# Kernel tuning notes

Measured on AMD Instinct MI355X. Metric: run time of the kernel, lower is better.

The kernel has to match this reference:

```python
import jax, jax.numpy as jnp
import numpy as np

MANTISA_BIT = 8.0  # mantisa_bit init arg


def conv3d(x, w, b, stride=1, pad=1):
    # x: [N,C,D,H,W], w: [O,I,kD,kH,kW]
    out = jax.lax.conv_general_dilated(
        x, w,
        window_strides=(stride, stride, stride),
        padding=[(pad, pad)] * 3,
        dimension_numbers=("NCDHW", "OIDHW", "NCDHW"),
    )
    return out + b.reshape(1, -1, 1, 1, 1)


def bfp_quant(x, ch_exp, m_bits):
    # Block floating point: shared per-channel exponent ch_exp [C],
    # signed mantissa with m_bits total bits. scale = 2^(m-1-exp);
    # q = clip(round(x*scale), -(2^(m-1)-1), 2^(m-1)-1)/scale
    scale = jnp.exp2(m_bits - 1.0 - ch_exp).reshape(1, -1, 1, 1, 1)
    lim = 2.0 ** (m_bits - 1.0) - 1.0
    return jnp.clip(jnp.round(x * scale), -lim, lim) / scale


def setup_inputs() -> dict:
    key = jax.random.key(0)
    ks = jax.random.split(key, 7)
    N, C_in, C_out, T, H, W, K = 8, 64, 64, 16, 56, 56, 3
    x = jax.random.normal(ks[0], (N, C_in, T, H, W), jnp.float32)
    w1 = jax.random.normal(ks[1], (C_out, C_in, K, K, K), jnp.float32) * 0.05
    b1 = jax.random.normal(ks[2], (C_out,), jnp.float32) * 0.05
    w2 = jax.random.normal(ks[3], (C_out, C_out, K, K, K), jnp.float32) * 0.05
    b2 = jax.random.normal(ks[4], (C_out,), jnp.float32) * 0.05
    # offline-optimized per-channel shared exponents (opt_exp_act_list[0], [1])
    exp1 = jax.random.randint(ks[5], (C_out,), 2, 6).astype(jnp.float32)
    exp2 = jax.random.randint(ks[6], (C_out,), 2, 6).astype(jnp.float32)
    return {"x": x, "w1": w1, "b1": b1, "w2": w2, "b2": b2,
            "exp1": exp1, "exp2": exp2}


def reference(x, w1, b1, w2, b2, exp1, exp2):
    # conv1 -> BFP quant -> ReLU
    res = conv3d(x, w1, b1)
    res = jax.nn.relu(bfp_quant(res, exp1, MANTISA_BIT))
    # conv2 -> BFP quant
    res = conv3d(res, w2, b2)
    res = bfp_quant(res, exp2, MANTISA_BIT)
    # identity shortcut (downsample=False) quantized with opt_exp_act_list[1]
    x_q = bfp_quant(x, exp2, MANTISA_BIT)
    return jax.nn.relu(x_q + res)
```

## Files before the change

kernel.cpp:

```cpp
#include <hip/hip_runtime.h>
#include <hip/hip_bf16.h>

#define Nn 8
#define Cc 64
#define Tt 16
#define Hh 56
#define Ww 56

typedef __bf16 bf16x8 __attribute__((ext_vector_type(8)));
typedef float f32x4 __attribute__((ext_vector_type(4)));
typedef unsigned short u16;
typedef unsigned int u32;

__device__ __forceinline__ u16 f32_to_bf16(float f) {
    u32 u = __float_as_uint(f);
    u32 r = (u + 0x7FFFu + ((u >> 16) & 1u)) >> 16;
    return (u16)r;
}
__device__ __forceinline__ float bf16_to_f32(u16 h) {
    return __uint_as_float(((u32)h) << 16);
}

__device__ __forceinline__ void gload16(const void* gsrc, void* lds) {
    __builtin_amdgcn_global_load_lds(
        (const __attribute__((address_space(1))) u32*)gsrc,
        (__attribute__((address_space(3))) u32*)lds, 16, 0, 0);
}

__global__ __launch_bounds__(256) void prep_w_kernel(
    const float* __restrict__ w1, const float* __restrict__ w2,
    u16* __restrict__ w1h, u16* __restrict__ w1l,
    u16* __restrict__ w2h, u16* __restrict__ w2l,
    u16* __restrict__ zpage)
{
    int idx = blockIdx.x * 256 + threadIdx.x;
    if (idx >= 221184) {
        ((uint4*)zpage)[idx - 221184] = make_uint4(0, 0, 0, 0);
        return;
    }
    int conv = idx / 110592;
    int rem  = idx % 110592;
    int tap  = rem >> 12;
    int co   = (rem >> 6) & 63;
    int ci   = rem & 63;
    const float* w = conv ? w2 : w1;
    float v = w[co * 1728 + ci * 27 + tap];
    u16 hi = f32_to_bf16(v);
    u16 lo = f32_to_bf16(v - bf16_to_f32(hi));
    int dst = tap * 4096 + co * 64 + ci;
    if (conv) { w2h[dst] = hi; w2l[dst] = lo; }
    else      { w1h[dst] = hi; w1l[dst] = lo; }
}

__global__ __launch_bounds__(256) void split_x_kernel(
    const float* __restrict__ x, u16* __restrict__ xh, u16* __restrict__ xl)
{
    __shared__ float tile[Cc][Hh + 1];
    const int tid = threadIdx.x;
    const int bid = blockIdx.x;
    const int h = bid % Hh;
    const int t = (bid / Hh) % Tt;
    const int n = bid / (Hh * Tt);
    for (int it = 0; it < 14; ++it) {
        int id = it * 256 + tid;
        int ci = id / Ww, w = id % Ww;
        tile[ci][w] = x[(((size_t)(n * Cc + ci) * Tt + t) * Hh + h) * Ww + w];
    }
    __syncthreads();
    const size_t obase = (size_t)bid * (Ww * Cc);
    for (int it = 0; it < 7; ++it) {
        int j = it * 256 + tid;
        int w = j >> 5, ci0 = (j & 31) << 1;
        float f0 = tile[ci0][w], f1 = tile[ci0 + 1][w];
        u16 h0 = f32_to_bf16(f0), h1 = f32_to_bf16(f1);
        u16 l0 = f32_to_bf16(f0 - bf16_to_f32(h0));
        u16 l1 = f32_to_bf16(f1 - bf16_to_f32(h1));
        size_t o = obase + (size_t)w * Cc + ci0;
        *(ushort2*)(xh + o) = make_ushort2(h0, h1);
        *(ushort2*)(xl + o) = make_ushort2(l0, l1);
    }
}

#define SLICE_B 3712
#define C1_BOFF 81920
#define C1_SMEM (81920 + 73728)
#define C2_BOFF 40960
#define C2_SMEM 81920

__device__ __forceinline__ const bf16x8* frag_ptr(const char* base, int row, int g) {
    int col = (g * 16) ^ (((row >> 1) & 3) << 4);
    return (const bf16x8*)(base + row * 64 + col);
}

__global__ __launch_bounds__(512, 2) void conv1_mfma_kernel(
    const u16* __restrict__ xh, const u16* __restrict__ xl,
    const u16* __restrict__ w1h, const u16* __restrict__ w1l,
    const float* __restrict__ b1, const float* __restrict__ e1,
    const u16* __restrict__ zpage, u16* __restrict__ res1)
{
    __shared__ __align__(16) char smem[C1_SMEM];
    char* As = smem;
    char* Bs = smem + C1_BOFF;

    const int tid = threadIdx.x;
    const int l = tid & 63, wid = tid >> 6;
    const int g = l >> 4, r15 = l & 15;
    const int wbase = tid & ~63;
    const int bid = (blockIdx.x & 7) * 112 + (blockIdx.x >> 3);
    const int hb = bid % 7;
    const int t  = (bid / 7) % Tt;
    const int n  = bid / (7 * Tt);
    const int h0 = hb * 8;

    f32x4 acc[4][4] = {};

#pragma unroll 1
    for (int cih = 0; cih < 2; ++cih) {
#pragma unroll 1
      for (int kd = 0; kd < 3; ++kd) {
        const int td = t + kd - 1;
        if (td < 0 || td >= Tt) continue;
        __builtin_amdgcn_sched_barrier(0);
        __builtin_amdgcn_s_barrier();
        __builtin_amdgcn_sched_barrier(0);
        {
          const size_t tdbase = (size_t)(n * Tt + td) * ((size_t)Hh * Ww * Cc);
#pragma unroll
          for (int it = 0; it < 10; ++it) {
            int fi = it * 512 + tid;
            int u = fi / 232, c = fi - u * 232;
            int r = c >> 2, slot = c & 3;
            int s = u >> 1, half = u & 1;
            int hh = h0 - 1 + s;
            int slog = slot ^ ((r >> 1) & 3);
            const u16* src = (half ? xl : xh) + tdbase
                + ((size_t)hh * Ww + (r - 1)) * Cc + cih * 32 + slog * 8;
            bool valid = (fi < 4640) & (hh >= 0) & (hh < Hh) & (r >= 1) & (r <= Ww);
            if (!valid) src = zpage;
            gload16(src, As + (it * 512 + wbase) * 16);
          }
        }
        {
#pragma unroll
          for (int it = 0; it < 9; ++it) {
            int fi = it * 512 + tid;
            int u = fi >> 8, c = fi & 255;
            int co = c >> 2, slot = c & 3;
            int slog = slot ^ ((co >> 1) & 3);
            int hl = (u >= 9), tap9 = u - 9 * hl;
            const u16* src = (hl ? w1l : w1h)
                + (kd * 9 + tap9) * 4096 + co * 64 + cih * 32 + slog * 8;
            gload16(src, Bs + (it * 512 + wbase) * 16);
          }
        }
        asm volatile("s_waitcnt vmcnt(0)" ::: "memory");
        __builtin_amdgcn_s_barrier();
        __builtin_amdgcn_sched_barrier(0);
        const char* Ab0 = As + (size_t)wid * 2 * SLICE_B;
#pragma unroll
        for (int kh = 0; kh < 3; ++kh) {
          const char* Ab = Ab0 + (size_t)kh * 2 * SLICE_B;
#pragma unroll
          for (int kw = 0; kw < 3; ++kw) {
            const int tap9 = kh * 3 + kw;
            bf16x8 ah[4], al[4], bh[4], bl[4];
#pragma unroll
            for (int m = 0; m < 4; ++m) {
              int row = r15 + 16 * m + kw;
              ah[m] = *frag_ptr(Ab, row, g);
              al[m] = *frag_ptr(Ab + SLICE_B, row, g);
            }
#pragma unroll
            for (int nt = 0; nt < 4; ++nt) {
              int co = r15 + 16 * nt;
              bh[nt] = *frag_ptr(Bs + tap9 * 4096, co, g);
              bl[nt] = *frag_ptr(Bs + (9 + tap9) * 4096, co, g);
            }
#pragma unroll
            for (int m = 0; m < 4; ++m)
#pragma unroll
              for (int nt = 0; nt < 4; ++nt) {
                acc[m][nt] = __builtin_amdgcn_mfma_f32_16x16x32_bf16(ah[m], bh[nt], acc[m][nt], 0, 0, 0);
                acc[m][nt] = __builtin_amdgcn_mfma_f32_16x16x32_bf16(al[m], bh[nt], acc[m][nt], 0, 0, 0);
                acc[m][nt] = __builtin_amdgcn_mfma_f32_16x16x32_bf16(ah[m], bl[nt], acc[m][nt], 0, 0, 0);
              }
          }
        }
      }
    }
    const int h = h0 + wid;
    const size_t rowbase = ((size_t)(n * Tt + t) * Hh + h) * ((size_t)Ww * Cc);
#pragma unroll
    for (int nt = 0; nt < 4; ++nt) {
      int co = 16 * nt + r15;
      float e = e1[co];
      float sc = exp2f(7.0f - e), inv = exp2f(e - 7.0f);
      float bias = b1[co];
#pragma unroll
      for (int m = 0; m < 4; ++m)
#pragma unroll
        for (int j = 0; j < 4; ++j) {
          int w = 16 * m + 4 * g + j;
          if (w < Ww) {
            float v = acc[m][nt][j] + bias;
            float q = rintf(v * sc);
            q = fminf(fmaxf(q, -127.f), 127.f);
            v = fmaxf(q * inv, 0.0f);
            res1[rowbase + (size_t)w * Cc + co] = f32_to_bf16(v);
          }
        }
    }
}

__global__ __launch_bounds__(512, 2) void conv2_mfma_kernel(
    const u16* __restrict__ a, const u16* __restrict__ w2h,
    const float* __restrict__ b2, const float* __restrict__ e2,
    const float* __restrict__ x, const u16* __restrict__ zpage,
    float* __restrict__ out)
{
    __shared__ __align__(16) char smem[C2_SMEM];
    char* As = smem;
    char* Bs = smem + C2_BOFF;

    const int tid = threadIdx.x;
    const int l = tid & 63, wid = tid >> 6;
    const int g = l >> 4, r15 = l & 15;
    const int wbase = tid & ~63;
    const int bid = (blockIdx.x & 7) * 112 + (blockIdx.x >> 3);
    const int hb = bid % 7;
    const int t  = (bid / 7) % Tt;
    const int n  = bid / (7 * Tt);
    const int h0 = hb * 8;

    f32x4 acc[4][4] = {};

#pragma unroll 1
    for (int cih = 0; cih < 2; ++cih) {
#pragma unroll 1
      for (int kd = 0; kd < 3; ++kd) {
        const int td = t + kd - 1;
        if (td < 0 || td >= Tt) continue;
        __builtin_amdgcn_sched_barrier(0);
        __builtin_amdgcn_s_barrier();
        __builtin_amdgcn_sched_barrier(0);
        {
          const size_t tdbase = (size_t)(n * Tt + td) * ((size_t)Hh * Ww * Cc);
#pragma unroll
          for (int it = 0; it < 5; ++it) {
            int fi = it * 512 + tid;
            int u = fi / 232, c = fi - u * 232;
            int r = c >> 2, slot = c & 3;
            int hh = h0 - 1 + u;
            int slog = slot ^ ((r >> 1) & 3);
            const u16* src = a + tdbase
                + ((size_t)hh * Ww + (r - 1)) * Cc + cih * 32 + slog * 8;
            bool valid = (fi < 2320) & (hh >= 0) & (hh < Hh) & (r >= 1) & (r <= Ww);
            if (!valid) src = zpage;
            gload16(src, As + (it * 512 + wbase) * 16);
          }
        }
        {
#pragma unroll
          for (int it = 0; it < 5; ++it) {
            int fi = it * 512 + tid;
            int u = fi >> 8, c = fi & 255;
            int co = c >> 2, slot = c & 3;
            int slog = slot ^ ((co >> 1) & 3);
            const u16* src = w2h + (kd * 9 + u) * 4096 + co * 64 + cih * 32 + slog * 8;
            if (fi >= 2304) src = zpage;
            gload16(src, Bs + (it * 512 + wbase) * 16);
          }
        }
        asm volatile("s_waitcnt vmcnt(0)" ::: "memory");
        __builtin_amdgcn_s_barrier();
        __builtin_amdgcn_sched_barrier(0);
        const char* Ab0 = As + (size_t)wid * SLICE_B;
#pragma unroll
        for (int kh = 0; kh < 3; ++kh) {
          const char* Ab = Ab0 + (size_t)kh * SLICE_B;
#pragma unroll
          for (int kw = 0; kw < 3; ++kw) {
            const int tap9 = kh * 3 + kw;
            bf16x8 af[4], bh[4];
#pragma unroll
            for (int m = 0; m < 4; ++m) {
              int row = r15 + 16 * m + kw;
              af[m] = *frag_ptr(Ab, row, g);
            }
#pragma unroll
            for (int nt = 0; nt < 4; ++nt) {
              int co = r15 + 16 * nt;
              bh[nt] = *frag_ptr(Bs + tap9 * 4096, co, g);
            }
#pragma unroll
            for (int m = 0; m < 4; ++m)
#pragma unroll
              for (int nt = 0; nt < 4; ++nt)
                acc[m][nt] = __builtin_amdgcn_mfma_f32_16x16x32_bf16(af[m], bh[nt], acc[m][nt], 0, 0, 0);
          }
        }
      }
    }
    const int h = h0 + wid;
#pragma unroll
    for (int nt = 0; nt < 4; ++nt) {
      int co = 16 * nt + r15;
      float e = e2[co];
      float sc = exp2f(7.0f - e), inv = exp2f(e - 7.0f);
      float bias = b2[co];
#pragma unroll
      for (int m = 0; m < 4; ++m)
#pragma unroll
        for (int j = 0; j < 4; ++j) {
          int w = 16 * m + 4 * g + j;
          if (w < Ww) {
            float v = acc[m][nt][j] + bias;
            float q = rintf(v * sc);
            q = fminf(fmaxf(q, -127.f), 127.f);
            v = q * inv;
            size_t xi = (((size_t)(n * Cc + co) * Tt + t) * Hh + h) * Ww + w;
            float xv = x[xi];
            float qx = rintf(xv * sc);
            qx = fminf(fmaxf(qx, -127.f), 127.f);
            out[xi] = fmaxf(qx * inv + v, 0.0f);
          }
        }
    }
}

extern "C" void kernel_launch(void* const* d_in, const int* in_sizes, int n_in,
                              void* d_out, int out_size, void* d_ws, size_t ws_size,
                              hipStream_t stream) {
    const float* x  = (const float*)d_in[0];
    const float* w1 = (const float*)d_in[1];
    const float* b1 = (const float*)d_in[2];
    const float* w2 = (const float*)d_in[3];
    const float* b2 = (const float*)d_in[4];
    const float* e1 = (const float*)d_in[5];
    const float* e2 = (const float*)d_in[6];

    const size_t NE = 25690112;
    u16* xh = (u16*)d_out;
    u16* xl = xh + NE;
    char* ws = (char*)d_ws;
    u16* w1h = (u16*)(ws);
    u16* w1l = (u16*)(ws + 221184);
    u16* w2h = (u16*)(ws + 442368);
    u16* w2l = (u16*)(ws + 663552);
    u16* zpage = (u16*)(ws + 884736);
    u16* res1  = (u16*)(ws + 888832);

    prep_w_kernel<<<865, 256, 0, stream>>>(w1, w2, w1h, w1l, w2h, w2l, zpage);
    split_x_kernel<<<Nn * Tt * Hh, 256, 0, stream>>>(x, xh, xl);
    const int nwg = Nn * Tt * 7;
    conv1_mfma_kernel<<<nwg, 512, 0, stream>>>(xh, xl, w1h, w1l, b1, e1, zpage, res1);
    conv2_mfma_kernel<<<nwg, 512, 0, stream>>>(res1, w2h, b2, e2, x, zpage, (float*)d_out);
}
```

Baseline: 411.8 us.

## Split conv1 tiles along width and stage hi/lo weights in two passes

Conv1 now gives each workgroup a 28-wide half row instead of the full 56 width, which doubles the grid to 1792 workgroups. LDS per block shrinks because the input slab is smaller and only one of the hi/lo weight halves is resident at a time. The lo-weight pass reloads the weights into the same LDS buffer after an extra barrier and reuses the A tile. The aim is better occupancy and less padded wasted MFMA work (56 widths no longer padded to 64), at the cost of extra barriers, duplicated halo loads and reloading the weights per workgroup.

```diff
diff --git a/kernel.cpp b/kernel.cpp
--- a/kernel.cpp
+++ b/kernel.cpp
@@ -81,13 +81,15 @@
     }
 }
 
+#define S1B   2176
+#define A1_B  (20 * S1B)
+#define B1_B  (9 * 4096)
+#define C1_SMEM (A1_B + B1_B)
 #define SLICE_B 3712
-#define C1_BOFF 81920
-#define C1_SMEM (81920 + 73728)
 #define C2_BOFF 40960
 #define C2_SMEM 81920
 
-__device__ __forceinline__ const bf16x8* frag_ptr(const char* base, int row, int g) {
+__device__ __forceinline__ const bf16x8* frag_ptr2(const char* base, int row, int g) {
     int col = (g * 16) ^ (((row >> 1) & 3) << 4);
     return (const bf16x8*)(base + row * 64 + col);
 }
@@ -100,7 +102,161 @@
 {
     __shared__ __align__(16) char smem[C1_SMEM];
     char* As = smem;
-    char* Bs = smem + C1_BOFF;
+    char* Bs = smem + A1_B;
+
+    const int tid = threadIdx.x;
+    const int l = tid & 63, wid = tid >> 6;
+    const int g = l >> 4, r15 = l & 15;
+    const int wbase = tid & ~63;
+    const int bid = (blockIdx.x & 7) * 224 + (blockIdx.x >> 3);
+    const int w0 = (bid & 1) * 28;
+    const int r2 = bid >> 1;
+    const int hb = r2 % 7;
+    const int t  = (r2 / 7) % Tt;
+    const int n  = r2 / (7 * Tt);
+    const int h0 = hb * 8;
+
+    f32x4 acc[2][4] = {};
+
+#pragma unroll 1
+    for (int cih = 0; cih < 2; ++cih) {
+#pragma unroll 1
+      for (int kd = 0; kd < 3; ++kd) {
+        const int td = t + kd - 1;
+        if (td < 0 || td >= Tt) continue;
+        __builtin_amdgcn_sched_barrier(0);
+        __builtin_amdgcn_s_barrier();
+        __builtin_amdgcn_sched_barrier(0);
+        {
+          const size_t tdbase = (size_t)(n * Tt + td) * ((size_t)Hh * Ww * Cc);
+#pragma unroll
+          for (int it = 0; it < 6; ++it) {
+            int fi = it * 512 + tid;
+            int u = fi / 136, c = fi - u * 136;
+            int r = c >> 2, slot = c & 3;
+            int s = u >> 1, half = u & 1;
+            int hh = h0 - 1 + s;
+            int pos = w0 - 1 + r;
+            int slog = slot ^ ((r >> 1) & 3);
+            const u16* src = (half ? xl : xh) + tdbase
+                + ((size_t)hh * Ww + pos) * Cc + cih * 32 + slog * 8;
+            bool valid = (fi < 2720) & (hh >= 0) & (hh < Hh) & (pos >= 0) & (pos < Ww);
+            if (!valid) src = zpage;
+            if (fi < 2720) gload16(src, As + (it * 512 + wbase) * 16);
+          }
+        }
+        {
+#pragma unroll
+          for (int it = 0; it < 5; ++it) {
+            int fi = it * 512 + tid;
+            int u = fi >> 8, c = fi & 255;
+            int co = c >> 2, slot = c & 3;
+            int slog = slot ^ ((co >> 1) & 3);
+            const u16* src = w1h + (kd * 9 + u) * 4096 + co * 64 + cih * 32 + slog * 8;
+            if (fi < 2304) gload16(src, Bs + (it * 512 + wbase) * 16);
+          }
+        }
+        asm volatile("s_waitcnt vmcnt(0)" ::: "memory");
+        __builtin_amdgcn_s_barrier();
+        __builtin_amdgcn_sched_barrier(0);
+        const char* Ab0 = As + (size_t)wid * 2 * S1B;
+#pragma unroll
+        for (int kh = 0; kh < 3; ++kh) {
+          const char* Ab = Ab0 + (size_t)kh * 2 * S1B;
+#pragma unroll
+          for (int kw = 0; kw < 3; ++kw) {
+            const int tap9 = kh * 3 + kw;
+            bf16x8 ah[2], al[2], bh[4];
+#pragma unroll
+            for (int m = 0; m < 2; ++m) {
+              int row = r15 + 16 * m + kw;
+              ah[m] = *frag_ptr2(Ab, row, g);
+              al[m] = *frag_ptr2(Ab + S1B, row, g);
+            }
+#pragma unroll
+            for (int nt = 0; nt < 4; ++nt)
+              bh[nt] = *frag_ptr2(Bs + tap9 * 4096, r15 + 16 * nt, g);
+#pragma unroll
+            for (int m = 0; m < 2; ++m)
+#pragma unroll
+              for (int nt = 0; nt < 4; ++nt) {
+                acc[m][nt] = __builtin_amdgcn_mfma_f32_16x16x32_bf16(ah[m], bh[nt], acc[m][nt], 0, 0, 0);
+                acc[m][nt] = __builtin_amdgcn_mfma_f32_16x16x32_bf16(al[m], bh[nt], acc[m][nt], 0, 0, 0);
+              }
+          }
+        }
+        __builtin_amdgcn_sched_barrier(0);
+        __builtin_amdgcn_s_barrier();
+        __builtin_amdgcn_sched_barrier(0);
+        {
+#pragma unroll
+          for (int it = 0; it < 5; ++it) {
+            int fi = it * 512 + tid;
+            int u = fi >> 8, c = fi & 255;
+            int co = c >> 2, slot = c & 3;
+            int slog = slot ^ ((co >> 1) & 3);
+            const u16* src = w1l + (kd * 9 + u) * 4096 + co * 64 + cih * 32 + slog * 8;
+            if (fi < 2304) gload16(src, Bs + (it * 512 + wbase) * 16);
+          }
+        }
+        asm volatile("s_waitcnt vmcnt(0)" ::: "memory");
+        __builtin_amdgcn_s_barrier();
+        __builtin_amdgcn_sched_barrier(0);
+#pragma unroll
+        for (int kh = 0; kh < 3; ++kh) {
+          const char* Ab = Ab0 + (size_t)kh * 2 * S1B;
+#pragma unroll
+          for (int kw = 0; kw < 3; ++kw) {
+            const int tap9 = kh * 3 + kw;
+            bf16x8 ah[2], bl[4];
+#pragma unroll
+            for (int m = 0; m < 2; ++m)
+              ah[m] = *frag_ptr2(Ab, r15 + 16 * m + kw, g);
+#pragma unroll
+            for (int nt = 0; nt < 4; ++nt)
+              bl[nt] = *frag_ptr2(Bs + tap9 * 4096, r15 + 16 * nt, g);
+#pragma unroll
+            for (int m = 0; m < 2; ++m)
+#pragma unroll
+              for (int nt = 0; nt < 4; ++nt)
+                acc[m][nt] = __builtin_amdgcn_mfma_f32_16x16x32_bf16(ah[m], bl[nt], acc[m][nt], 0, 0, 0);
+          }
+        }
+      }
+    }
+    const int h = h0 + wid;
+    const size_t rowbase = ((size_t)(n * Tt + t) * Hh + h) * ((size_t)Ww * Cc);
+#pragma unroll
+    for (int nt = 0; nt < 4; ++nt) {
+      int co = 16 * nt + r15;
+      float e = e1[co];
+      float sc = exp2f(7.0f - e), inv = exp2f(e - 7.0f);
+      float bias = b1[co];
+#pragma unroll
+      for (int m = 0; m < 2; ++m)
+#pragma unroll
+        for (int j = 0; j < 4; ++j) {
+          int wl = 16 * m + 4 * g + j;
+          if (wl < 28) {
+            float v = acc[m][nt][j] + bias;
+            float q = rintf(v * sc);
+            q = fminf(fmaxf(q, -127.f), 127.f);
+            v = fmaxf(q * inv, 0.0f);
+            res1[rowbase + (size_t)(w0 + wl) * Cc + co] = f32_to_bf16(v);
+          }
+        }
+    }
+}
+
+__global__ __launch_bounds__(512, 2) void conv2_mfma_kernel(
+    const u16* __restrict__ a, const u16* __restrict__ w2h,
+    const float* __restrict__ b2, const float* __restrict__ e2,
+    const float* __restrict__ x, const u16* __restrict__ zpage,
+    float* __restrict__ out)
+{
+    __shared__ __align__(16) char smem[C2_SMEM];
+    char* As = smem;
+    char* Bs = smem + C2_BOFF;
 
     const int tid = threadIdx.x;
     const int l = tid & 63, wid = tid >> 6;
@@ -126,126 +282,6 @@
         {
           const size_t tdbase = (size_t)(n * Tt + td) * ((size_t)Hh * Ww * Cc);
 #pragma unroll
-          for (int it = 0; it < 10; ++it) {
-            int fi = it * 512 + tid;
-            int u = fi / 232, c = fi - u * 232;
-            int r = c >> 2, slot = c & 3;
-            int s = u >> 1, half = u & 1;
-            int hh = h0 - 1 + s;
-            int slog = slot ^ ((r >> 1) & 3);
-            const u16* src = (half ? xl : xh) + tdbase
-                + ((size_t)hh * Ww + (r - 1)) * Cc + cih * 32 + slog * 8;
-            bool valid = (fi < 4640) & (hh >= 0) & (hh < Hh) & (r >= 1) & (r <= Ww);
-            if (!valid) src = zpage;
-            gload16(src, As + (it * 512 + wbase) * 16);
-          }
-        }
-        {
-#pragma unroll
-          for (int it = 0; it < 9; ++it) {
-            int fi = it * 512 + tid;
-            int u = fi >> 8, c = fi & 255;
-            int co = c >> 2, slot = c & 3;
-            int slog = slot ^ ((co >> 1) & 3);
-            int hl = (u >= 9), tap9 = u - 9 * hl;
-            const u16* src = (hl ? w1l : w1h)
-                + (kd * 9 + tap9) * 4096 + co * 64 + cih * 32 + slog * 8;
-            gload16(src, Bs + (it * 512 + wbase) * 16);
-          }
-        }
-        asm volatile("s_waitcnt vmcnt(0)" ::: "memory");
-        __builtin_amdgcn_s_barrier();
-        __builtin_amdgcn_sched_barrier(0);
-        const char* Ab0 = As + (size_t)wid * 2 * SLICE_B;
-#pragma unroll
-        for (int kh = 0; kh < 3; ++kh) {
-          const char* Ab = Ab0 + (size_t)kh * 2 * SLICE_B;
-#pragma unroll
-          for (int kw = 0; kw < 3; ++kw) {
-            const int tap9 = kh * 3 + kw;
-            bf16x8 ah[4], al[4], bh[4], bl[4];
-#pragma unroll
-            for (int m = 0; m < 4; ++m) {
-              int row = r15 + 16 * m + kw;
-              ah[m] = *frag_ptr(Ab, row, g);
-              al[m] = *frag_ptr(Ab + SLICE_B, row, g);
-            }
-#pragma unroll
-            for (int nt = 0; nt < 4; ++nt) {
-              int co = r15 + 16 * nt;
-              bh[nt] = *frag_ptr(Bs + tap9 * 4096, co, g);
-              bl[nt] = *frag_ptr(Bs + (9 + tap9) * 4096, co, g);
-            }
-#pragma unroll
-            for (int m = 0; m < 4; ++m)
-#pragma unroll
-              for (int nt = 0; nt < 4; ++nt) {
-                acc[m][nt] = __builtin_amdgcn_mfma_f32_16x16x32_bf16(ah[m], bh[nt], acc[m][nt], 0, 0, 0);
-                acc[m][nt] = __builtin_amdgcn_mfma_f32_16x16x32_bf16(al[m], bh[nt], acc[m][nt], 0, 0, 0);
-                acc[m][nt] = __builtin_amdgcn_mfma_f32_16x16x32_bf16(ah[m], bl[nt], acc[m][nt], 0, 0, 0);
-              }
-          }
-        }
-      }
-    }
-    const int h = h0 + wid;
-    const size_t rowbase = ((size_t)(n * Tt + t) * Hh + h) * ((size_t)Ww * Cc);
-#pragma unroll
-    for (int nt = 0; nt < 4; ++nt) {
-      int co = 16 * nt + r15;
-      float e = e1[co];
-      float sc = exp2f(7.0f - e), inv = exp2f(e - 7.0f);
-      float bias = b1[co];
-#pragma unroll
-      for (int m = 0; m < 4; ++m)
-#pragma unroll
-        for (int j = 0; j < 4; ++j) {
-          int w = 16 * m + 4 * g + j;
-          if (w < Ww) {
-            float v = acc[m][nt][j] + bias;
-            float q = rintf(v * sc);
-            q = fminf(fmaxf(q, -127.f), 127.f);
-            v = fmaxf(q * inv, 0.0f);
-            res1[rowbase + (size_t)w * Cc + co] = f32_to_bf16(v);
-          }
-        }
-    }
-}
-
-__global__ __launch_bounds__(512, 2) void conv2_mfma_kernel(
-    const u16* __restrict__ a, const u16* __restrict__ w2h,
-    const float* __restrict__ b2, const float* __restrict__ e2,
-    const float* __restrict__ x, const u16* __restrict__ zpage,
-    float* __restrict__ out)
-{
-    __shared__ __align__(16) char smem[C2_SMEM];
-    char* As = smem;
-    char* Bs = smem + C2_BOFF;
-
-    const int tid = threadIdx.x;
-    const int l = tid & 63, wid = tid >> 6;
-    const int g = l >> 4, r15 = l & 15;
-    const int wbase = tid & ~63;
-    const int bid = (blockIdx.x & 7) * 112 + (blockIdx.x >> 3);
-    const int hb = bid % 7;
-    const int t  = (bid / 7) % Tt;
-    const int n  = bid / (7 * Tt);
-    const int h0 = hb * 8;
-
-    f32x4 acc[4][4] = {};
-
-#pragma unroll 1
-    for (int cih = 0; cih < 2; ++cih) {
-#pragma unroll 1
-      for (int kd = 0; kd < 3; ++kd) {
-        const int td = t + kd - 1;
-        if (td < 0 || td >= Tt) continue;
-        __builtin_amdgcn_sched_barrier(0);
-        __builtin_amdgcn_s_barrier();
-        __builtin_amdgcn_sched_barrier(0);
-        {
-          const size_t tdbase = (size_t)(n * Tt + td) * ((size_t)Hh * Ww * Cc);
-#pragma unroll
           for (int it = 0; it < 5; ++it) {
             int fi = it * 512 + tid;
             int u = fi / 232, c = fi - u * 232;
@@ -283,15 +319,11 @@
             const int tap9 = kh * 3 + kw;
             bf16x8 af[4], bh[4];
 #pragma unroll
-            for (int m = 0; m < 4; ++m) {
-              int row = r15 + 16 * m + kw;
-              af[m] = *frag_ptr(Ab, row, g);
-            }
-#pragma unroll
-            for (int nt = 0; nt < 4; ++nt) {
-              int co = r15 + 16 * nt;
-              bh[nt] = *frag_ptr(Bs + tap9 * 4096, co, g);
-            }
+            for (int m = 0; m < 4; ++m)
+              af[m] = *frag_ptr2(Ab, r15 + 16 * m + kw, g);
+#pragma unroll
+            for (int nt = 0; nt < 4; ++nt)
+              bh[nt] = *frag_ptr2(Bs + tap9 * 4096, r15 + 16 * nt, g);
 #pragma unroll
             for (int m = 0; m < 4; ++m)
 #pragma unroll
@@ -352,7 +384,6 @@
 
     prep_w_kernel<<<865, 256, 0, stream>>>(w1, w2, w1h, w1l, w2h, w2l, zpage);
     split_x_kernel<<<Nn * Tt * Hh, 256, 0, stream>>>(x, xh, xl);
-    const int nwg = Nn * Tt * 7;
-    conv1_mfma_kernel<<<nwg, 512, 0, stream>>>(xh, xl, w1h, w1l, b1, e1, zpage, res1);
-    conv2_mfma_kernel<<<nwg, 512, 0, stream>>>(res1, w2h, b2, e2, x, zpage, (float*)d_out);
-}
+    conv1_mfma_kernel<<<1792, 512, 0, stream>>>(xh, xl, w1h, w1l, b1, e1, zpage, res1);
+    conv2_mfma_kernel<<<896, 512, 0, stream>>>(res1, w2h, b2, e2, x, zpage, (float*)d_out);
+}
```

After: 416.6 us. About the same (+1.2%).

## Drop x low-part split, use 32x32 MFMA, double-buffer conv1 input tiles

Applied to the files above, without the earlier changes.

Conv1 no longer splits the input x into high and low bf16 parts, so only the high part is stored and loaded. That removes one third of conv1's MFMAs and half of its activation traffic, at the cost of reduced accuracy for conv1. Both convolutions move from 16x16x32 to 32x32x16 MFMA tiles. Conv1 also double-buffers its activation tiles in LDS to overlap the next load with compute, which drops occupancy to one block per CU.

```diff
diff --git a/kernel.cpp b/kernel.cpp
--- a/kernel.cpp
+++ b/kernel.cpp
@@ -8,7 +8,7 @@
 #define Ww 56
 
 typedef __bf16 bf16x8 __attribute__((ext_vector_type(8)));
-typedef float f32x4 __attribute__((ext_vector_type(4)));
+typedef float f32x16 __attribute__((ext_vector_type(16)));
 typedef unsigned short u16;
 typedef unsigned int u32;
 
@@ -53,7 +53,7 @@
 }
 
 __global__ __launch_bounds__(256) void split_x_kernel(
-    const float* __restrict__ x, u16* __restrict__ xh, u16* __restrict__ xl)
+    const float* __restrict__ x, u16* __restrict__ xh)
 {
     __shared__ float tile[Cc][Hh + 1];
     const int tid = threadIdx.x;
@@ -71,40 +71,36 @@
     for (int it = 0; it < 7; ++it) {
         int j = it * 256 + tid;
         int w = j >> 5, ci0 = (j & 31) << 1;
-        float f0 = tile[ci0][w], f1 = tile[ci0 + 1][w];
-        u16 h0 = f32_to_bf16(f0), h1 = f32_to_bf16(f1);
-        u16 l0 = f32_to_bf16(f0 - bf16_to_f32(h0));
-        u16 l1 = f32_to_bf16(f1 - bf16_to_f32(h1));
-        size_t o = obase + (size_t)w * Cc + ci0;
-        *(ushort2*)(xh + o) = make_ushort2(h0, h1);
-        *(ushort2*)(xl + o) = make_ushort2(l0, l1);
+        u16 h0 = f32_to_bf16(tile[ci0][w]);
+        u16 h1 = f32_to_bf16(tile[ci0 + 1][w]);
+        *(ushort2*)(xh + obase + (size_t)w * Cc + ci0) = make_ushort2(h0, h1);
     }
 }
 
 #define SLICE_B 3712
-#define C1_BOFF 81920
+#define A1_BUF 40960
+#define B1_OFF (2 * A1_BUF)
 #define C1_SMEM (81920 + 73728)
 #define C2_BOFF 40960
 #define C2_SMEM 81920
 
-__device__ __forceinline__ const bf16x8* frag_ptr(const char* base, int row, int g) {
-    int col = (g * 16) ^ (((row >> 1) & 3) << 4);
+__device__ __forceinline__ const bf16x8* frag_ptr(const char* base, int row, int slot) {
+    int col = (slot * 16) ^ (((row >> 1) & 3) << 4);
     return (const bf16x8*)(base + row * 64 + col);
 }
 
-__global__ __launch_bounds__(512, 2) void conv1_mfma_kernel(
-    const u16* __restrict__ xh, const u16* __restrict__ xl,
+__global__ __launch_bounds__(512, 1) void conv1_mfma_kernel(
+    const u16* __restrict__ xh,
     const u16* __restrict__ w1h, const u16* __restrict__ w1l,
     const float* __restrict__ b1, const float* __restrict__ e1,
     const u16* __restrict__ zpage, u16* __restrict__ res1)
 {
     __shared__ __align__(16) char smem[C1_SMEM];
-    char* As = smem;
-    char* Bs = smem + C1_BOFF;
+    char* Bs = smem + B1_OFF;
 
     const int tid = threadIdx.x;
     const int l = tid & 63, wid = tid >> 6;
-    const int g = l >> 4, r15 = l & 15;
+    const int l31 = l & 31, hi5 = l >> 5;
     const int wbase = tid & ~63;
     const int bid = (blockIdx.x & 7) * 112 + (blockIdx.x >> 3);
     const int hb = bid % 7;
@@ -112,37 +108,32 @@
     const int n  = bid / (7 * Tt);
     const int h0 = hb * 8;
 
-    f32x4 acc[4][4] = {};
-
-#pragma unroll 1
-    for (int cih = 0; cih < 2; ++cih) {
-#pragma unroll 1
-      for (int kd = 0; kd < 3; ++kd) {
+    f32x16 acc[2][2] = {};
+
+    char* Acur = smem;
+    char* Anxt = smem + A1_BUF;
+
+    auto ISSUE_A = [&](int cih, int kd, char* dst) {
         const int td = t + kd - 1;
-        if (td < 0 || td >= Tt) continue;
-        __builtin_amdgcn_sched_barrier(0);
-        __builtin_amdgcn_s_barrier();
-        __builtin_amdgcn_sched_barrier(0);
-        {
-          const size_t tdbase = (size_t)(n * Tt + td) * ((size_t)Hh * Ww * Cc);
-#pragma unroll
-          for (int it = 0; it < 10; ++it) {
+        const bool tdv = (td >= 0 && td < Tt);
+        const size_t tdbase = (size_t)(n * Tt + (tdv ? td : 0)) * ((size_t)Hh * Ww * Cc);
+#pragma unroll
+        for (int it = 0; it < 5; ++it) {
             int fi = it * 512 + tid;
             int u = fi / 232, c = fi - u * 232;
             int r = c >> 2, slot = c & 3;
-            int s = u >> 1, half = u & 1;
-            int hh = h0 - 1 + s;
+            int hh = h0 - 1 + u;
             int slog = slot ^ ((r >> 1) & 3);
-            const u16* src = (half ? xl : xh) + tdbase
+            const u16* src = xh + tdbase
                 + ((size_t)hh * Ww + (r - 1)) * Cc + cih * 32 + slog * 8;
-            bool valid = (fi < 4640) & (hh >= 0) & (hh < Hh) & (r >= 1) & (r <= Ww);
+            bool valid = tdv & (fi < 2320) & (hh >= 0) & (hh < Hh) & (r >= 1) & (r <= Ww);
             if (!valid) src = zpage;
-            gload16(src, As + (it * 512 + wbase) * 16);
-          }
-        }
-        {
-#pragma unroll
-          for (int it = 0; it < 9; ++it) {
+            gload16(src, dst + (it * 512 + wbase) * 16);
+        }
+    };
+    auto ISSUE_B = [&](int cih, int kd) {
+#pragma unroll
+        for (int it = 0; it < 9; ++it) {
             int fi = it * 512 + tid;
             int u = fi >> 8, c = fi & 255;
             int co = c >> 2, slot = c & 3;
@@ -151,64 +142,90 @@
             const u16* src = (hl ? w1l : w1h)
                 + (kd * 9 + tap9) * 4096 + co * 64 + cih * 32 + slog * 8;
             gload16(src, Bs + (it * 512 + wbase) * 16);
-          }
-        }
-        asm volatile("s_waitcnt vmcnt(0)" ::: "memory");
+        }
+    };
+
+    ISSUE_A(0, 0, Acur);
+    ISSUE_B(0, 0);
+    asm volatile("s_waitcnt vmcnt(0)" ::: "memory");
+    __builtin_amdgcn_s_barrier();
+    __builtin_amdgcn_sched_barrier(0);
+
+#pragma unroll 1
+    for (int i = 0; i < 6; ++i) {
+        if (i < 5) ISSUE_A((i + 1) / 3, (i + 1) % 3, Anxt);
+        __builtin_amdgcn_sched_barrier(0);
+        const char* Ab0 = Acur + (size_t)wid * SLICE_B;
+#pragma unroll
+        for (int kh = 0; kh < 3; ++kh) {
+            const char* Ab = Ab0 + (size_t)kh * SLICE_B;
+#pragma unroll
+            for (int kw = 0; kw < 3; ++kw) {
+                const int tap9 = kh * 3 + kw;
+                bf16x8 a[2][2], bh[2][2], bl[2][2];
+#pragma unroll
+                for (int m = 0; m < 2; ++m)
+#pragma unroll
+                    for (int kk = 0; kk < 2; ++kk)
+                        a[m][kk] = *frag_ptr(Ab, l31 + 32 * m + kw, kk * 2 + hi5);
+#pragma unroll
+                for (int nt = 0; nt < 2; ++nt)
+#pragma unroll
+                    for (int kk = 0; kk < 2; ++kk) {
+                        int co = l31 + 32 * nt;
+                        bh[nt][kk] = *frag_ptr(Bs + tap9 * 4096, co, kk * 2 + hi5);
+                        bl[nt][kk] = *frag_ptr(Bs + (9 + tap9) * 4096, co, kk * 2 + hi5);
+                    }
+#pragma unroll
+                for (int m = 0; m < 2; ++m)
+#pragma unroll
+                    for (int nt = 0; nt < 2; ++nt)
+#pragma unroll
+                        for (int kk = 0; kk < 2; ++kk)
+                            acc[m][nt] = __builtin_amdgcn_mfma_f32_32x32x16_bf16(
+                                a[m][kk], bh[nt][kk], acc[m][nt], 0, 0, 0);
+#pragma unroll
+                for (int m = 0; m < 2; ++m)
+#pragma unroll
+                    for (int nt = 0; nt < 2; ++nt)
+#pragma unroll
+                        for (int kk = 0; kk < 2; ++kk)
+                            acc[m][nt] = __builtin_amdgcn_mfma_f32_32x32x16_bf16(
+                                a[m][kk], bl[nt][kk], acc[m][nt], 0, 0, 0);
+            }
+        }
+        __builtin_amdgcn_sched_barrier(0);
         __builtin_amdgcn_s_barrier();
-        __builtin_amdgcn_sched_barrier(0);
-        const char* Ab0 = As + (size_t)wid * 2 * SLICE_B;
-#pragma unroll
-        for (int kh = 0; kh < 3; ++kh) {
-          const char* Ab = Ab0 + (size_t)kh * 2 * SLICE_B;
-#pragma unroll
-          for (int kw = 0; kw < 3; ++kw) {
-            const int tap9 = kh * 3 + kw;
-            bf16x8 ah[4], al[4], bh[4], bl[4];
-#pragma unroll
-            for (int m = 0; m < 4; ++m) {
-              int row = r15 + 16 * m + kw;
-              ah[m] = *frag_ptr(Ab, row, g);
-              al[m] = *frag_ptr(Ab + SLICE_B, row, g);
-            }
-#pragma unroll
-            for (int nt = 0; nt < 4; ++nt) {
-              int co = r15 + 16 * nt;
-              bh[nt] = *frag_ptr(Bs + tap9 * 4096, co, g);
-              bl[nt] = *frag_ptr(Bs + (9 + tap9) * 4096, co, g);
-            }
-#pragma unroll
-            for (int m = 0; m < 4; ++m)
-#pragma unroll
-              for (int nt = 0; nt < 4; ++nt) {
-                acc[m][nt] = __builtin_amdgcn_mfma_f32_16x16x32_bf16(ah[m], bh[nt], acc[m][nt], 0, 0, 0);
-                acc[m][nt] = __builtin_amdgcn_mfma_f32_16x16x32_bf16(al[m], bh[nt], acc[m][nt], 0, 0, 0);
-                acc[m][nt] = __builtin_amdgcn_mfma_f32_16x16x32_bf16(ah[m], bl[nt], acc[m][nt], 0, 0, 0);
-              }
-          }
-        }
-      }
-    }
+        if (i < 5) {
+            ISSUE_B((i + 1) / 3, (i + 1) % 3);
+            asm volatile("s_waitcnt vmcnt(0)" ::: "memory");
+            __builtin_amdgcn_s_barrier();
+            __builtin_amdgcn_sched_barrier(0);
+        }
+        char* tmp = Acur; Acur = Anxt; Anxt = tmp;
+    }
+
     const int h = h0 + wid;
     const size_t rowbase = ((size_t)(n * Tt + t) * Hh + h) * ((size_t)Ww * Cc);
 #pragma unroll
-    for (int nt = 0; nt < 4; ++nt) {
-      int co = 16 * nt + r15;
-      float e = e1[co];
-      float sc = exp2f(7.0f - e), inv = exp2f(e - 7.0f);
-      float bias = b1[co];
-#pragma unroll
-      for (int m = 0; m < 4; ++m)
-#pragma unroll
-        for (int j = 0; j < 4; ++j) {
-          int w = 16 * m + 4 * g + j;
-          if (w < Ww) {
-            float v = acc[m][nt][j] + bias;
-            float q = rintf(v * sc);
-            q = fminf(fmaxf(q, -127.f), 127.f);
-            v = fmaxf(q * inv, 0.0f);
-            res1[rowbase + (size_t)w * Cc + co] = f32_to_bf16(v);
-          }
-        }
+    for (int nt = 0; nt < 2; ++nt) {
+        int co = 32 * nt + l31;
+        float e = e1[co];
+        float sc = exp2f(7.0f - e), inv = exp2f(e - 7.0f);
+        float bias = b1[co];
+#pragma unroll
+        for (int m = 0; m < 2; ++m)
+#pragma unroll
+            for (int reg = 0; reg < 16; ++reg) {
+                int w = 32 * m + (reg & 3) + 8 * (reg >> 2) + 4 * hi5;
+                if (w < Ww) {
+                    float v = acc[m][nt][reg] + bias;
+                    float q = rintf(v * sc);
+                    q = fminf(fmaxf(q, -127.f), 127.f);
+                    v = fmaxf(q * inv, 0.0f);
+                    res1[rowbase + (size_t)w * Cc + co] = f32_to_bf16(v);
+                }
+            }
     }
 }
 
@@ -224,7 +241,7 @@
 
     const int tid = threadIdx.x;
     const int l = tid & 63, wid = tid >> 6;
-    const int g = l >> 4, r15 = l & 15;
+    const int l31 = l & 31, hi5 = l >> 5;
     const int wbase = tid & ~63;
     const int bid = (blockIdx.x & 7) * 112 + (blockIdx.x >> 3);
     const int hb = bid % 7;
@@ -232,7 +249,7 @@
     const int n  = bid / (7 * Tt);
     const int h0 = hb * 8;
 
-    f32x4 acc[4][4] = {};
+    f32x16 acc[2][2] = {};
 
 #pragma unroll 1
     for (int cih = 0; cih < 2; ++cih) {
@@ -281,40 +298,43 @@
 #pragma unroll
           for (int kw = 0; kw < 3; ++kw) {
             const int tap9 = kh * 3 + kw;
-            bf16x8 af[4], bh[4];
-#pragma unroll
-            for (int m = 0; m < 4; ++m) {
-              int row = r15 + 16 * m + kw;
-              af[m] = *frag_ptr(Ab, row, g);
-            }
-#pragma unroll
-            for (int nt = 0; nt < 4; ++nt) {
-              int co = r15 + 16 * nt;
-              bh[nt] = *frag_ptr(Bs + tap9 * 4096, co, g);
-            }
-#pragma unroll
-            for (int m = 0; m < 4; ++m)
-#pragma unroll
-              for (int nt = 0; nt < 4; ++nt)
-                acc[m][nt] = __builtin_amdgcn_mfma_f32_16x16x32_bf16(af[m], bh[nt], acc[m][nt], 0, 0, 0);
+            bf16x8 a2[2][2], bh[2][2];
+#pragma unroll
+            for (int m = 0; m < 2; ++m)
+#pragma unroll
+              for (int kk = 0; kk < 2; ++kk)
+                a2[m][kk] = *frag_ptr(Ab, l31 + 32 * m + kw, kk * 2 + hi5);
+#pragma unroll
+            for (int nt = 0; nt < 2; ++nt)
+#pragma unroll
+              for (int kk = 0; kk < 2; ++kk)
+                bh[nt][kk] = *frag_ptr(Bs + tap9 * 4096, l31 + 32 * nt, kk * 2 + hi5);
+#pragma unroll
+            for (int m = 0; m < 2; ++m)
+#pragma unroll
+              for (int nt = 0; nt < 2; ++nt)
+#pragma unroll
+                for (int kk = 0; kk < 2; ++kk)
+                  acc[m][nt] = __builtin_amdgcn_mfma_f32_32x32x16_bf16(
+                      a2[m][kk], bh[nt][kk], acc[m][nt], 0, 0, 0);
           }
         }
       }
     }
     const int h = h0 + wid;
 #pragma unroll
-    for (int nt = 0; nt < 4; ++nt) {
-      int co = 16 * nt + r15;
+    for (int nt = 0; nt < 2; ++nt) {
+      int co = 32 * nt + l31;
       float e = e2[co];
       float sc = exp2f(7.0f - e), inv = exp2f(e - 7.0f);
       float bias = b2[co];
 #pragma unroll
-      for (int m = 0; m < 4; ++m)
-#pragma unroll
-        for (int j = 0; j < 4; ++j) {
-          int w = 16 * m + 4 * g + j;
+      for (int m = 0; m < 2; ++m)
+#pragma unroll
+        for (int reg = 0; reg < 16; ++reg) {
+          int w = 32 * m + (reg & 3) + 8 * (reg >> 2) + 4 * hi5;
           if (w < Ww) {
-            float v = acc[m][nt][j] + bias;
+            float v = acc[m][nt][reg] + bias;
             float q = rintf(v * sc);
             q = fminf(fmaxf(q, -127.f), 127.f);
             v = q * inv;
@@ -339,9 +359,7 @@
     const float* e1 = (const float*)d_in[5];
     const float* e2 = (const float*)d_in[6];
 
-    const size_t NE = 25690112;
     u16* xh = (u16*)d_out;
-    u16* xl = xh + NE;
     char* ws = (char*)d_ws;
     u16* w1h = (u16*)(ws);
     u16* w1l = (u16*)(ws + 221184);
@@ -351,8 +369,7 @@
     u16* res1  = (u16*)(ws + 888832);
 
     prep_w_kernel<<<865, 256, 0, stream>>>(w1, w2, w1h, w1l, w2h, w2l, zpage);
-    split_x_kernel<<<Nn * Tt * Hh, 256, 0, stream>>>(x, xh, xl);
-    const int nwg = Nn * Tt * 7;
-    conv1_mfma_kernel<<<nwg, 512, 0, stream>>>(xh, xl, w1h, w1l, b1, e1, zpage, res1);
-    conv2_mfma_kernel<<<nwg, 512, 0, stream>>>(res1, w2h, b2, e2, x, zpage, (float*)d_out);
-}
+    split_x_kernel<<<Nn * Tt * Hh, 256, 0, stream>>>(x, xh);
+    conv1_mfma_kernel<<<896, 512, 0, stream>>>(xh, w1h, w1l, b1, e1, zpage, res1);
+    conv2_mfma_kernel<<<896, 512, 0, stream>>>(res1, w2h, b2, e2, x, zpage, (float*)d_out);
+}
```

After: 354.6 us. -13.9%, faster.
